# Kernel tuning notes

Hardware: AMD Instinct MI355X
Metric: run time of the kernel (lower is better)

Reference implementation:

```python
import jax, jax.numpy as jnp
import numpy as np

TWO_PI = 6.283185307179586


def setup_inputs() -> dict:
    key = jax.random.key(0)
    k1, k2, k3, k4, k5, k6 = jax.random.split(key, 6)
    B, T, D = 2, 8192, 1024
    x = jax.random.normal(k1, (B, T, D), dtype=jnp.float32)
    # nn.Linear weights are [out, in]; init with small scale like torch default
    s = 1.0 / np.sqrt(D)
    Wk = jax.random.uniform(k2, (D, D), jnp.float32, -s, s)
    Wv = jax.random.uniform(k3, (D, D), jnp.float32, -s, s)
    Wo = jax.random.uniform(k4, (D, D), jnp.float32, -s, s)
    # random phasor frequencies in [0, 2*pi)
    freqs = jax.random.uniform(k5, (D,), jnp.float32, 0.0, TWO_PI)
    return {"x": x, "Wk": Wk, "Wv": Wv, "Wo": Wo, "freqs": freqs}


def reference(x, Wk, Wv, Wo, freqs):
    B, T, C = x.shape
    # k projection is computed in the original forward but never used downstream
    k_real = x @ Wk.T  # [B,T,D] (dead value, kept for fidelity)
    v_real = x @ Wv.T  # [B,T,D]
    v = v_real.astype(jnp.complex64)
    # rotors: per-position unit phasors exp(i * t * freqs), shape [T, D]
    t = jnp.arange(T, dtype=jnp.float32)
    rotors = jnp.exp(1j * (t[:, None] * freqs[None, :])).astype(jnp.complex64)
    # bind each value with its rotor and accumulate causally (O(N) memory trace)
    memory_trace = jnp.cumsum(v * rotors[None, :, :], axis=1)  # [B,T,D] complex64
    # retrieve by unbinding with the conjugate rotor; take the real component
    retrieved = jnp.real(memory_trace * jnp.conj(rotors)[None, :, :])  # [B,T,D]
    return retrieved @ Wo.T
```

## Files before the change

kernel.cpp:

```cpp
#include <hip/hip_runtime.h>
#include <hip/hip_bf16.h>


#define B_  2
#define T_  8192
#define D_  1024
#define BT_ 16384
#define CS_ 64
#define NCHUNK_ 128

typedef __attribute__((ext_vector_type(4))) float f32x4;
typedef __attribute__((ext_vector_type(8))) short bf16x8;

static __device__ inline unsigned short f2bf(float f) {
    union { float f; unsigned int u; } a;
    a.f = f;
    unsigned int u = a.u;
    return (unsigned short)((u + 0x7FFFu + ((u >> 16) & 1u)) >> 16);
}
static __device__ inline float bf2f(unsigned short h) {
    union { unsigned int u; float f; } a;
    a.u = ((unsigned int)h) << 16;
    return a.f;
}

__global__ __launch_bounds__(256) void cast_all(const float* __restrict__ x,
                                                const float* __restrict__ Wv,
                                                const float* __restrict__ Wo,
                                                unsigned short* __restrict__ xb,
                                                unsigned short* __restrict__ wvb,
                                                unsigned short* __restrict__ wob) {
    const int nx = BT_ * D_ / 4;
    const int nw = D_ * D_ / 4;
    int i = blockIdx.x * 256 + threadIdx.x;
    const float4* src;
    unsigned short* dst;
    int j;
    if (i < nx)            { src = (const float4*)x;  dst = xb;  j = i; }
    else if (i < nx + nw)  { src = (const float4*)Wv; dst = wvb; j = i - nx; }
    else                   { src = (const float4*)Wo; dst = wob; j = i - nx - nw; }
    float4 v = src[j];
    ushort4 o;
    o.x = f2bf(v.x); o.y = f2bf(v.y); o.z = f2bf(v.z); o.w = f2bf(v.w);
    ((ushort4*)dst)[j] = o;
}

template <bool BF16OUT, bool FUSE_SUMS>
__global__ __launch_bounds__(512, 2) void gemm_bt(const short* __restrict__ A,
                                                  const short* __restrict__ Bm,
                                                  void* __restrict__ Cout,
                                                  const float* __restrict__ freqs,
                                                  float* __restrict__ csum,
                                                  int M, int N, int K) {
    __shared__ short lds[65536];
    const int tid = threadIdx.x;
    const int lane = tid & 63;
    const int wave = tid >> 6;
    const int wm = wave >> 2, wn = wave & 3;

    const int nb = N >> 8;
    const int id = blockIdx.x;
    const int xcd = id & 7;
    const int slot = id >> 3;
    const int bn = (slot % nb) * 256;
    const int bm = (xcd * ((M >> 8) >> 3) + slot / nb) * 256;

    const int srow = lane >> 3;
    const int sg = lane & 7;
    const size_t cstep = (size_t)64 * K;
    const short* gA = A + (size_t)(bm + wave * 8 + srow) * K + ((sg ^ srow) * 8);
    const short* gB = Bm + (size_t)(bn + wave * 8 + srow) * K + ((sg ^ srow) * 8);

    auto stage1 = [&](int kt, int g) {
        const int c = g & 3;
        const short* src = ((g & 4) ? gB : gA) + c * cstep + kt * 64;
        short* dst = &lds[(kt & 1) * 32768 + ((g & 4) ? 16384 : 0) + c * 4096 + wave * 512];
        __builtin_amdgcn_global_load_lds(
            (const __attribute__((address_space(1))) void*)src,
            (__attribute__((address_space(3))) void*)dst, 16, 0, 0);
    };

    const int l15 = lane & 15;
    const int c4r = lane >> 4;
    const int swz0 = ((c4r) ^ (lane & 7)) * 8;
    const int swz1 = ((4 + c4r) ^ (lane & 7)) * 8;
    const int abase = (wm * 128 + l15) * 64;
    const int bbase = 16384 + (wn * 64 + l15) * 64;

    f32x4 acc[8][4] = {};

    stage1(0, 0); stage1(0, 1); stage1(0, 2); stage1(0, 3);
    stage1(0, 4); stage1(0, 5); stage1(0, 6); stage1(0, 7);
    stage1(1, 0); stage1(1, 2);
    stage1(1, 4); stage1(1, 5); stage1(1, 6); stage1(1, 7);
    asm volatile("s_waitcnt vmcnt(6)" ::: "memory");
    __builtin_amdgcn_sched_barrier(0);
    __builtin_amdgcn_s_barrier();

    const int NT = K >> 6;
#pragma unroll 1
    for (int t = 0; t < NT; ++t) {
        const int sb = (t & 1) * 32768;
        bf16x8 av[4][2], b01[2][2], b23[2][2];

#pragma unroll
        for (int ii = 0; ii < 4; ++ii) {
            av[ii][0] = *(const bf16x8*)&lds[sb + abase + ii * 1024 + swz0];
            av[ii][1] = *(const bf16x8*)&lds[sb + abase + ii * 1024 + swz1];
        }
#pragma unroll
        for (int j = 0; j < 2; ++j) {
            b01[j][0] = *(const bf16x8*)&lds[sb + bbase + j * 1024 + swz0];
            b01[j][1] = *(const bf16x8*)&lds[sb + bbase + j * 1024 + swz1];
        }
        if (t + 1 < NT) { stage1(t + 1, 1); stage1(t + 1, 3); }
        __builtin_amdgcn_s_barrier();
        asm volatile("s_waitcnt lgkmcnt(0)" ::: "memory");
        __builtin_amdgcn_sched_barrier(0);
        __builtin_amdgcn_s_setprio(1);
#pragma unroll
        for (int ks = 0; ks < 2; ++ks)
#pragma unroll
            for (int ii = 0; ii < 4; ++ii)
#pragma unroll
                for (int j = 0; j < 2; ++j)
                    acc[ii][j] = __builtin_amdgcn_mfma_f32_16x16x32_bf16(
                        av[ii][ks], b01[j][ks], acc[ii][j], 0, 0, 0);
        __builtin_amdgcn_s_setprio(0);
        __builtin_amdgcn_s_barrier();

#pragma unroll
        for (int j = 0; j < 2; ++j) {
            b23[j][0] = *(const bf16x8*)&lds[sb + bbase + (2 + j) * 1024 + swz0];
            b23[j][1] = *(const bf16x8*)&lds[sb + bbase + (2 + j) * 1024 + swz1];
        }
        if (t + 2 < NT) { stage1(t + 2, 0); stage1(t + 2, 2); }
        __builtin_amdgcn_s_barrier();
        asm volatile("s_waitcnt lgkmcnt(0)" ::: "memory");
        __builtin_amdgcn_sched_barrier(0);
        __builtin_amdgcn_s_setprio(1);
#pragma unroll
        for (int ks = 0; ks < 2; ++ks)
#pragma unroll
            for (int ii = 0; ii < 4; ++ii)
#pragma unroll
                for (int j = 0; j < 2; ++j)
                    acc[ii][2 + j] = __builtin_amdgcn_mfma_f32_16x16x32_bf16(
                        av[ii][ks], b23[j][ks], acc[ii][2 + j], 0, 0, 0);
        __builtin_amdgcn_s_setprio(0);
        __builtin_amdgcn_s_barrier();

#pragma unroll
        for (int ii = 0; ii < 4; ++ii) {
            av[ii][0] = *(const bf16x8*)&lds[sb + abase + (4 + ii) * 1024 + swz0];
            av[ii][1] = *(const bf16x8*)&lds[sb + abase + (4 + ii) * 1024 + swz1];
        }
        if (t + 2 < NT) { stage1(t + 2, 4); stage1(t + 2, 5); }
        __builtin_amdgcn_s_barrier();
        asm volatile("s_waitcnt lgkmcnt(0)" ::: "memory");
        __builtin_amdgcn_sched_barrier(0);
        __builtin_amdgcn_s_setprio(1);
#pragma unroll
        for (int ks = 0; ks < 2; ++ks)
#pragma unroll
            for (int ii = 0; ii < 4; ++ii)
#pragma unroll
                for (int j = 0; j < 2; ++j)
                    acc[4 + ii][2 + j] = __builtin_amdgcn_mfma_f32_16x16x32_bf16(
                        av[ii][ks], b23[j][ks], acc[4 + ii][2 + j], 0, 0, 0);
        __builtin_amdgcn_s_setprio(0);
        __builtin_amdgcn_s_barrier();

        if (t + 2 < NT) { stage1(t + 2, 6); stage1(t + 2, 7); }
        if (t + 2 < NT) asm volatile("s_waitcnt vmcnt(6)" ::: "memory");
        else            asm volatile("s_waitcnt vmcnt(0)" ::: "memory");
        __builtin_amdgcn_sched_barrier(0);
        __builtin_amdgcn_s_barrier();
        __builtin_amdgcn_s_setprio(1);
#pragma unroll
        for (int ks = 0; ks < 2; ++ks)
#pragma unroll
            for (int ii = 0; ii < 4; ++ii)
#pragma unroll
                for (int j = 0; j < 2; ++j)
                    acc[4 + ii][j] = __builtin_amdgcn_mfma_f32_16x16x32_bf16(
                        av[ii][ks], b01[j][ks], acc[4 + ii][j], 0, 0, 0);
        __builtin_amdgcn_s_setprio(0);
        __builtin_amdgcn_s_barrier();
    }

    const int row0 = c4r * 4;
#pragma unroll
    for (int i = 0; i < 8; ++i) {
#pragma unroll
        for (int j = 0; j < 4; ++j) {
            const int col = bn + wn * 64 + j * 16 + (lane & 15);
#pragma unroll
            for (int r = 0; r < 4; ++r) {
                const size_t row = (size_t)bm + wm * 128 + i * 16 + row0 + r;
                if constexpr (BF16OUT)
                    ((unsigned short*)Cout)[row * N + col] = f2bf(acc[i][j][r]);
                else
                    ((float*)Cout)[row * N + col] = acc[i][j][r];
            }
        }
    }

    if constexpr (FUSE_SUMS) {
        const int b = bm >> 13;
        const int trow = bm & 8191;
#pragma unroll
        for (int ig = 0; ig < 2; ++ig) {
            const int chunk = (trow >> 6) + wm * 2 + ig;
            const int t0 = trow + wm * 128 + ig * 64 + c4r * 4;
#pragma unroll
            for (int j = 0; j < 4; ++j) {
                const int d = bn + wn * 64 + j * 16 + (lane & 15);
                const float f = freqs[d];
                float ss, cc2;
                sincosf((float)t0 * f, &ss, &cc2);
                float s1, c1;
                sincosf(f, &s1, &c1);
                float c2 = c1 * c1 - s1 * s1, s2 = 2.f * c1 * s1;
                float c4 = c2 * c2 - s2 * s2, s4 = 2.f * c2 * s2;
                float c8 = c4 * c4 - s4 * s4, s8 = 2.f * c4 * s4;
                float c12 = c8 * c4 - s8 * s4, s12 = s8 * c4 + c8 * s4;
                float c13 = c12 * c1 - s12 * s1, s13 = s12 * c1 + c12 * s1;
                float ar = 0.f, ai = 0.f;
                float cr = cc2, sr2 = ss;
#pragma unroll
                for (int ii = 0; ii < 4; ++ii) {
                    const int i = ig * 4 + ii;
#pragma unroll
                    for (int r = 0; r < 4; ++r) {
                        const float w = acc[i][j][r];
                        ar = fmaf(w, cr, ar); ai = fmaf(w, sr2, ai);
                        const float ec = (r < 3) ? c1 : c13;
                        const float es = (r < 3) ? s1 : s13;
                        const float nc = cr * ec - sr2 * es;
                        const float ns = sr2 * ec + cr * es;
                        cr = nc; sr2 = ns;
                    }
                }
                ar += __shfl_xor(ar, 16); ai += __shfl_xor(ai, 16);
                ar += __shfl_xor(ar, 32); ai += __shfl_xor(ai, 32);
                if (c4r == 0)
                    *(float2*)(csum + (((size_t)b * NCHUNK_ + chunk) * D_ + d) * 2) =
                        make_float2(ar, ai);
            }
        }
    }
}

__global__ __launch_bounds__(256) void scan_pass2(float* __restrict__ csum) {
    const int g = blockIdx.x * 256 + threadIdx.x;
    const int b = g / D_;
    const int d = g % D_;
    float2* cs = (float2*)csum;
    const size_t base = (size_t)b * NCHUNK_ * D_ + d;
    float pr = 0.f, pi = 0.f;
    for (int cc = 0; cc < NCHUNK_; cc += 32) {
        float2 buf[32];
#pragma unroll
        for (int k = 0; k < 32; ++k) buf[k] = cs[base + (size_t)(cc + k) * D_];
#pragma unroll
        for (int k = 0; k < 32; ++k) {
            float r = buf[k].x, im = buf[k].y;
            buf[k] = make_float2(pr, pi);
            pr += r; pi += im;
        }
#pragma unroll
        for (int k = 0; k < 32; ++k) cs[base + (size_t)(cc + k) * D_] = buf[k];
    }
}

__global__ __launch_bounds__(256) void scan_pass3(const unsigned short* __restrict__ v,
                                                  const float* __restrict__ freqs,
                                                  const float* __restrict__ csum,
                                                  unsigned short* __restrict__ ret) {
    const int chunk = blockIdx.x;
    const int d0 = blockIdx.y * 512 + threadIdx.x * 2;
    const int b = blockIdx.z;

    float fr[2], s[2], c[2], sf[2], cf[2], ar[2], ai[2];
    {
        float2 f2 = *(const float2*)(freqs + d0);
        fr[0] = f2.x; fr[1] = f2.y;
    }
    const float t0f = (float)(chunk * CS_);
#pragma unroll
    for (int k = 0; k < 2; ++k) {
        sincosf(t0f * fr[k], &s[k], &c[k]);
        sincosf(fr[k], &sf[k], &cf[k]);
    }
    {
        const float4 o = *(const float4*)(csum + (((size_t)b * NCHUNK_ + chunk) * D_ + d0) * 2);
        ar[0] = o.x; ai[0] = o.y; ar[1] = o.z; ai[1] = o.w;
    }
    const unsigned int* vp = (const unsigned int*)(v + ((size_t)b * T_ + chunk * CS_) * D_ + d0);
    unsigned int* rp = (unsigned int*)(ret + ((size_t)b * T_ + chunk * CS_) * D_ + d0);
    for (int tb = 0; tb < CS_; tb += 8) {
        unsigned int w[8];
#pragma unroll
        for (int u = 0; u < 8; ++u) w[u] = vp[(size_t)(tb + u) * (D_ / 2)];
#pragma unroll
        for (int u = 0; u < 8; ++u) {
            float wv[2], o[2];
            wv[0] = bf2f((unsigned short)w[u]);
            wv[1] = bf2f((unsigned short)(w[u] >> 16));
#pragma unroll
            for (int k = 0; k < 2; ++k) {
                ar[k] = fmaf(wv[k], c[k], ar[k]);
                ai[k] = fmaf(wv[k], s[k], ai[k]);
                o[k] = ar[k] * c[k] + ai[k] * s[k];
                float nc = c[k] * cf[k] - s[k] * sf[k];
                float ns = s[k] * cf[k] + c[k] * sf[k];
                c[k] = nc; s[k] = ns;
            }
            rp[(size_t)(tb + u) * (D_ / 2)] =
                (unsigned int)f2bf(o[0]) | ((unsigned int)f2bf(o[1]) << 16);
        }
    }
}

extern "C" void kernel_launch(void* const* d_in, const int* in_sizes, int n_in,
                              void* d_out, int out_size, void* d_ws, size_t ws_size,
                              hipStream_t stream) {
    const float* x     = (const float*)d_in[0];
    const float* Wv    = (const float*)d_in[2];
    const float* Wo    = (const float*)d_in[3];
    const float* freqs = (const float*)d_in[4];
    float* out = (float*)d_out;

    char* ws = (char*)d_ws;
    unsigned short* x_bf  = (unsigned short*)ws;
    unsigned short* Wv_bf = (unsigned short*)(ws + 33554432);
    unsigned short* Wo_bf = (unsigned short*)(ws + 35651584);
    unsigned short* ret   = (unsigned short*)(ws + 37748736);
    float*          csum  = (float*)(ws + 71303168);
    unsigned short* v_bf = (unsigned short*)d_out;

    cast_all<<<(BT_ * D_ / 4 + 2 * D_ * D_ / 4) / 256, 256, 0, stream>>>(
        x, Wv, Wo, x_bf, Wv_bf, Wo_bf);

    gemm_bt<true, true><<<(BT_ / 256) * (D_ / 256), 512, 0, stream>>>(
        (const short*)x_bf, (const short*)Wv_bf, (void*)v_bf, freqs, csum, BT_, D_, D_);

    scan_pass2<<<(B_ * D_) / 256, 256, 0, stream>>>(csum);
    dim3 p3grid(NCHUNK_, D_ / 512, B_);
    scan_pass3<<<p3grid, 256, 0, stream>>>(v_bf, freqs, csum, ret);

    gemm_bt<false, false><<<(BT_ / 256) * (D_ / 256), 512, 0, stream>>>(
        (const short*)ret, (const short*)Wo_bf, (void*)out, nullptr, nullptr, BT_, D_, D_);
}
```

Before: 235.0 us.

## Halve scan chunk size, widen cast stores, reorder GEMM prefetch, reuse workspace

Scan chunk size drops from 64 to 32 rows, doubling the number of chunks. This gives the pass-3 scan more parallel blocks and shorter serial recurrences, at the cost of more partial sums for pass 2. The cast kernel now converts 8 floats per thread with a 16-byte store. The GEMM prologue loads both k-tiles in full and all prefetches target t+2, rescheduled across the loop phases with a new vmcnt threshold. The retrieved buffer now aliases the x_bf workspace region to cut the workspace footprint.

```diff
diff --git a/kernel.cpp b/kernel.cpp
--- a/kernel.cpp
+++ b/kernel.cpp
@@ -6,11 +6,12 @@
 #define T_  8192
 #define D_  1024
 #define BT_ 16384
-#define CS_ 64
-#define NCHUNK_ 128
+#define CS_ 32
+#define NCHUNK_ 256
 
 typedef __attribute__((ext_vector_type(4))) float f32x4;
 typedef __attribute__((ext_vector_type(8))) short bf16x8;
+typedef __attribute__((ext_vector_type(8))) unsigned short ushort8;
 
 static __device__ inline unsigned short f2bf(float f) {
     union { float f; unsigned int u; } a;
@@ -30,8 +31,8 @@
                                                 unsigned short* __restrict__ xb,
                                                 unsigned short* __restrict__ wvb,
                                                 unsigned short* __restrict__ wob) {
-    const int nx = BT_ * D_ / 4;
-    const int nw = D_ * D_ / 4;
+    const int nx = BT_ * D_ / 8;
+    const int nw = D_ * D_ / 8;
     int i = blockIdx.x * 256 + threadIdx.x;
     const float4* src;
     unsigned short* dst;
@@ -39,10 +40,12 @@
     if (i < nx)            { src = (const float4*)x;  dst = xb;  j = i; }
     else if (i < nx + nw)  { src = (const float4*)Wv; dst = wvb; j = i - nx; }
     else                   { src = (const float4*)Wo; dst = wob; j = i - nx - nw; }
-    float4 v = src[j];
-    ushort4 o;
-    o.x = f2bf(v.x); o.y = f2bf(v.y); o.z = f2bf(v.z); o.w = f2bf(v.w);
-    ((ushort4*)dst)[j] = o;
+    float4 a = src[j * 2];
+    float4 b = src[j * 2 + 1];
+    ushort8 o;
+    o[0] = f2bf(a.x); o[1] = f2bf(a.y); o[2] = f2bf(a.z); o[3] = f2bf(a.w);
+    o[4] = f2bf(b.x); o[5] = f2bf(b.y); o[6] = f2bf(b.z); o[7] = f2bf(b.w);
+    *(ushort8*)&dst[(size_t)j * 8] = o;
 }
 
 template <bool BF16OUT, bool FUSE_SUMS>
@@ -89,11 +92,11 @@
 
     f32x4 acc[8][4] = {};
 
-    stage1(0, 0); stage1(0, 1); stage1(0, 2); stage1(0, 3);
-    stage1(0, 4); stage1(0, 5); stage1(0, 6); stage1(0, 7);
-    stage1(1, 0); stage1(1, 2);
-    stage1(1, 4); stage1(1, 5); stage1(1, 6); stage1(1, 7);
-    asm volatile("s_waitcnt vmcnt(6)" ::: "memory");
+#pragma unroll
+    for (int g = 0; g < 8; ++g) stage1(0, g);
+#pragma unroll
+    for (int g = 0; g < 8; ++g) stage1(1, g);
+    asm volatile("s_waitcnt vmcnt(8)" ::: "memory");
     __builtin_amdgcn_sched_barrier(0);
     __builtin_amdgcn_s_barrier();
 
@@ -101,6 +104,7 @@
 #pragma unroll 1
     for (int t = 0; t < NT; ++t) {
         const int sb = (t & 1) * 32768;
+        const bool pf = (t + 2 < NT);
         bf16x8 av[4][2], b01[2][2], b23[2][2];
 
 #pragma unroll
@@ -113,7 +117,6 @@
             b01[j][0] = *(const bf16x8*)&lds[sb + bbase + j * 1024 + swz0];
             b01[j][1] = *(const bf16x8*)&lds[sb + bbase + j * 1024 + swz1];
         }
-        if (t + 1 < NT) { stage1(t + 1, 1); stage1(t + 1, 3); }
         __builtin_amdgcn_s_barrier();
         asm volatile("s_waitcnt lgkmcnt(0)" ::: "memory");
         __builtin_amdgcn_sched_barrier(0);
@@ -134,7 +137,7 @@
             b23[j][0] = *(const bf16x8*)&lds[sb + bbase + (2 + j) * 1024 + swz0];
             b23[j][1] = *(const bf16x8*)&lds[sb + bbase + (2 + j) * 1024 + swz1];
         }
-        if (t + 2 < NT) { stage1(t + 2, 0); stage1(t + 2, 2); }
+        if (pf) { stage1(t + 2, 0); stage1(t + 2, 2); }
         __builtin_amdgcn_s_barrier();
         asm volatile("s_waitcnt lgkmcnt(0)" ::: "memory");
         __builtin_amdgcn_sched_barrier(0);
@@ -155,7 +158,7 @@
             av[ii][0] = *(const bf16x8*)&lds[sb + abase + (4 + ii) * 1024 + swz0];
             av[ii][1] = *(const bf16x8*)&lds[sb + abase + (4 + ii) * 1024 + swz1];
         }
-        if (t + 2 < NT) { stage1(t + 2, 4); stage1(t + 2, 5); }
+        if (pf) { stage1(t + 2, 4); stage1(t + 2, 5); stage1(t + 2, 6); stage1(t + 2, 7); }
         __builtin_amdgcn_s_barrier();
         asm volatile("s_waitcnt lgkmcnt(0)" ::: "memory");
         __builtin_amdgcn_sched_barrier(0);
@@ -171,9 +174,9 @@
         __builtin_amdgcn_s_setprio(0);
         __builtin_amdgcn_s_barrier();
 
-        if (t + 2 < NT) { stage1(t + 2, 6); stage1(t + 2, 7); }
-        if (t + 2 < NT) asm volatile("s_waitcnt vmcnt(6)" ::: "memory");
-        else            asm volatile("s_waitcnt vmcnt(0)" ::: "memory");
+        if (pf) { stage1(t + 2, 1); stage1(t + 2, 3); }
+        if (pf) asm volatile("s_waitcnt vmcnt(8)" ::: "memory");
+        else    asm volatile("s_waitcnt vmcnt(0)" ::: "memory");
         __builtin_amdgcn_sched_barrier(0);
         __builtin_amdgcn_s_barrier();
         __builtin_amdgcn_s_setprio(1);
@@ -210,9 +213,9 @@
         const int b = bm >> 13;
         const int trow = bm & 8191;
 #pragma unroll
-        for (int ig = 0; ig < 2; ++ig) {
-            const int chunk = (trow >> 6) + wm * 2 + ig;
-            const int t0 = trow + wm * 128 + ig * 64 + c4r * 4;
+        for (int ig2 = 0; ig2 < 4; ++ig2) {
+            const int chunk = (trow >> 5) + wm * 4 + ig2;
+            const int t0 = trow + wm * 128 + ig2 * 32 + c4r * 4;
 #pragma unroll
             for (int j = 0; j < 4; ++j) {
                 const int d = bn + wn * 64 + j * 16 + (lane & 15);
@@ -229,8 +232,8 @@
                 float ar = 0.f, ai = 0.f;
                 float cr = cc2, sr2 = ss;
 #pragma unroll
-                for (int ii = 0; ii < 4; ++ii) {
-                    const int i = ig * 4 + ii;
+                for (int f2 = 0; f2 < 2; ++f2) {
+                    const int i = ig2 * 2 + f2;
 #pragma unroll
                     for (int r = 0; r < 4; ++r) {
                         const float w = acc[i][j][r];
@@ -336,11 +339,11 @@
     unsigned short* x_bf  = (unsigned short*)ws;
     unsigned short* Wv_bf = (unsigned short*)(ws + 33554432);
     unsigned short* Wo_bf = (unsigned short*)(ws + 35651584);
-    unsigned short* ret   = (unsigned short*)(ws + 37748736);
-    float*          csum  = (float*)(ws + 71303168);
+    float*          csum  = (float*)(ws + 37748736);
+    unsigned short* ret  = (unsigned short*)ws;
     unsigned short* v_bf = (unsigned short*)d_out;
 
-    cast_all<<<(BT_ * D_ / 4 + 2 * D_ * D_ / 4) / 256, 256, 0, stream>>>(
+    cast_all<<<(BT_ * D_ / 8 + 2 * D_ * D_ / 8) / 256, 256, 0, stream>>>(
         x, Wv, Wo, x_bf, Wv_bf, Wo_bf);
 
     gemm_bt<true, true><<<(BT_ / 256) * (D_ / 256), 512, 0, stream>>>(
```

Result: slower. 243.6 us (+3.7%).
